# Optimization experiments

Measured on AMD Instinct MI355X. Metric: run time of the kernel, lower is better.

Reference implementation:

```python
import jax, jax.numpy as jnp
import numpy as np
from jax.ops import segment_sum, segment_max

N_NODES = 100000
N_EDGES = 1600000
IN, HID, OUT = 256, 64, 40
NEG_SLOPE = 0.2  # DGL GATConv default


def setup_inputs() -> dict:
    key = jax.random.key(0)
    ks = jax.random.split(key, 12)
    feat = jax.random.normal(ks[0], (N_NODES, IN), dtype=jnp.float32)
    src = jax.random.randint(ks[1], (N_EDGES,), 0, N_NODES)
    dst = jax.random.randint(ks[2], (N_EDGES,), 0, N_NODES)
    def xavier(k, shape):
        fan = sum(shape)
        return jax.random.normal(k, shape, dtype=jnp.float32) * jnp.sqrt(2.0 / fan)
    return {
        "feat": feat, "src": src, "dst": dst,
        "W1": xavier(ks[3], (IN, HID)),  "b1": jnp.zeros((HID,), jnp.float32),
        "al1": xavier(ks[4], (HID,)),    "ar1": xavier(ks[5], (HID,)),
        "W2": xavier(ks[6], (HID, OUT)), "b2": jnp.zeros((OUT,), jnp.float32),
        "al2": xavier(ks[7], (OUT,)),    "ar2": xavier(ks[8], (OUT,)),
    }


def gat_layer(x, W, b, attn_l, attn_r, src, dst, n):
    # z: [N, F_out] projected features
    z = x @ W
    el = z @ attn_l          # [N] source attention logits
    er = z @ attn_r          # [N] destination attention logits
    e = jax.nn.leaky_relu(el[src] + er[dst], NEG_SLOPE)  # [E]
    # segment (per-destination) softmax over incoming edges
    m = segment_max(e, dst, num_segments=n)              # [N]
    w = jnp.exp(e - m[dst])                              # [E]
    s = segment_sum(w, dst, num_segments=n)              # [N]
    alpha = w / s[dst]                                   # [E]
    # scatter-add aggregation of alpha * z[src]
    out = segment_sum(alpha[:, None] * z[src], dst, num_segments=n)
    return out + b


def reference(feat, src, dst, W1, b1, al1, ar1, W2, b2, al2, ar2):
    n = feat.shape[0]
    h = gat_layer(feat, W1, b1, al1, ar1, src, dst, n)
    h = jax.nn.relu(h)  # dropout is identity in eval mode
    h = gat_layer(h, W2, b2, al2, ar2, src, dst, n)
    return jax.nn.log_softmax(h, axis=-1)  # [N, out_size]
```

## Files before the change

### kernel.cpp

```cpp
#include <hip/hip_runtime.h>
#include <math.h>

constexpr int NN   = 100000;
constexpr int NE   = 1600000;
constexpr int FIN  = 256;
constexpr int HID  = 64;
constexpr int FOUT = 40;
constexpr float SLOPE = 0.2f;
constexpr int NB    = (NN + 255) / 256;
constexpr int NBUCK = NB;
constexpr int TILE_A = 2048;
constexpr int NWG_A = (NE + TILE_A - 1) / TILE_A;
constexpr int AK = 264;

typedef short  short8  __attribute__((ext_vector_type(8)));
typedef float  floatx4 __attribute__((ext_vector_type(4)));

__device__ inline unsigned short f2bf(float x) {
    union { float f; unsigned int u; } c; c.f = x;
    unsigned int u = c.u;
    return (unsigned short)((u + 0x7FFF + ((u >> 16) & 1)) >> 16);
}

__device__ inline float readlane_f(float v, int l) {
    return __int_as_float(__builtin_amdgcn_readlane(__float_as_int(v), l));
}

__global__ __launch_bounds__(256) void w1t_kernel(
    const float* __restrict__ W1, unsigned short* __restrict__ W1T)
{
    int idx = blockIdx.x * 256 + threadIdx.x;
    if (idx < FIN * HID) {
        int k = idx >> 6, n = idx & 63;
        W1T[n * FIN + k] = f2bf(W1[idx]);
    }
}

__global__ __launch_bounds__(256) void gemm1_kernel(
    const float* __restrict__ feat, const unsigned short* __restrict__ W1T,
    const float* __restrict__ al, const float* __restrict__ ar,
    const int* __restrict__ dst, int* __restrict__ bcnt,
    _Float16* __restrict__ z, float* __restrict__ el, float* __restrict__ er)
{
    __shared__ unsigned short sBT[64 * AK];
    __shared__ int hist[NBUCK];
    const int t = threadIdx.x;
    const int ntile = blockIdx.x * 64;

    for (int i = t; i < NBUCK; i += 256) hist[i] = 0;
    #pragma unroll
    for (int i = 0; i < 8; ++i) {
        int g = t + 256 * i;
        int row = g >> 5, c8 = g & 31;
        *(uint4*)&sBT[row * AK + 8 * c8] = *(const uint4*)&W1T[row * FIN + 8 * c8];
    }
    __syncthreads();

    {
        int base = (blockIdx.x * 256 + t) * 4;
        if (base < NE) {
            const int4 d4 = *(const int4*)&dst[base];
            atomicAdd(&hist[d4.x >> 8], 1); atomicAdd(&hist[d4.y >> 8], 1);
            atomicAdd(&hist[d4.z >> 8], 1); atomicAdd(&hist[d4.w >> 8], 1);
        }
    }
    __syncthreads();
    for (int i = t; i < NBUCK; i += 256) {
        int hv = hist[i];
        if (hv) atomicAdd(&bcnt[i], hv);
    }

    const int w  = t >> 6;
    const int l  = t & 63;
    const int lr = l & 15;
    const int q  = l >> 4;
    const int m0 = 16 * w;

    int n = ntile + m0 + lr; if (n >= NN) n = NN - 1;
    const float* __restrict__ arow = feat + (size_t)n * FIN;

    floatx4 acc[4];
    #pragma unroll
    for (int tile = 0; tile < 4; ++tile) acc[tile] = 0.f;

    #pragma unroll
    for (int kc = 0; kc < 8; ++kc) {
        const int koff = kc * 32 + 8 * q;
        const float4 fa = *(const float4*)(arow + koff);
        const float4 fb = *(const float4*)(arow + koff + 4);
        short8 av;
        av[0] = (short)f2bf(fa.x); av[1] = (short)f2bf(fa.y);
        av[2] = (short)f2bf(fa.z); av[3] = (short)f2bf(fa.w);
        av[4] = (short)f2bf(fb.x); av[5] = (short)f2bf(fb.y);
        av[6] = (short)f2bf(fb.z); av[7] = (short)f2bf(fb.w);
        #pragma unroll
        for (int tile = 0; tile < 4; ++tile) {
            const short8 bv = *(const short8*)(sBT + (16 * tile + lr) * AK + koff);
            acc[tile] = __builtin_amdgcn_mfma_f32_16x16x32_bf16(av, bv, acc[tile], 0, 0, 0);
        }
    }

    float aln[4], arn[4];
    #pragma unroll
    for (int tile = 0; tile < 4; ++tile) {
        aln[tile] = al[16 * tile + lr];
        arn[tile] = ar[16 * tile + lr];
    }
    #pragma unroll
    for (int r = 0; r < 4; ++r) {
        int mg = ntile + m0 + 4 * q + r;
        float pl = 0.f, pr = 0.f;
        #pragma unroll
        for (int tile = 0; tile < 4; ++tile) {
            float zv = acc[tile][r];
            pl += zv * aln[tile]; pr += zv * arn[tile];
        }
        #pragma unroll
        for (int off = 8; off >= 1; off >>= 1) {
            pl += __shfl_xor(pl, off);
            pr += __shfl_xor(pr, off);
        }
        if (mg < NN) {
            #pragma unroll
            for (int tile = 0; tile < 4; ++tile)
                z[(size_t)mg * HID + 16 * tile + lr] = (_Float16)acc[tile][r];
            if (lr == 0) { el[mg] = pl; er[mg] = pr; }
        }
    }
}

__global__ __launch_bounds__(512) void scan_top_kernel(
    const int* __restrict__ bcnt, int* __restrict__ bofs, int* __restrict__ gcur)
{
    __shared__ int tmp[512];
    int t = threadIdx.x;
    int v = (t < NB) ? bcnt[t] : 0;
    tmp[t] = v; __syncthreads();
    for (int off = 1; off < 512; off <<= 1) {
        int x = (t >= off) ? tmp[t - off] : 0;
        __syncthreads();
        tmp[t] += x;
        __syncthreads();
    }
    int excl = tmp[t] - v;
    if (t < NB) { bofs[t] = excl; gcur[t] = excl; }
    if (t == NB - 1) bofs[NB] = excl + v;
}

__global__ __launch_bounds__(1024) void partitionA_kernel(
    const int* __restrict__ src, const int* __restrict__ dst,
    int* __restrict__ gcur, int* __restrict__ ebuck)
{
    __shared__ int hist[NBUCK];
    __shared__ int lcur[NBUCK];
    const int t = threadIdx.x;
    const int e0 = blockIdx.x * TILE_A;
    const int e1 = (e0 + TILE_A < NE) ? e0 + TILE_A : NE;

    for (int i = t; i < NBUCK; i += 1024) hist[i] = 0;
    __syncthreads();
    for (int e = e0 + t; e < e1; e += 1024)
        atomicAdd(&hist[dst[e] >> 8], 1);
    __syncthreads();
    for (int i = t; i < NBUCK; i += 1024) {
        int hv = hist[i];
        lcur[i] = hv ? atomicAdd(&gcur[i], hv) : 0;
    }
    __syncthreads();
    for (int e = e0 + t; e < e1; e += 1024) {
        int d = dst[e], s = src[e];
        int p = atomicAdd(&lcur[d >> 8], 1);
        ebuck[p] = (s << 8) | (d & 255);
    }
}

__global__ __launch_bounds__(1024) void partitionB_kernel(
    const int* __restrict__ bofs, const int* __restrict__ ebuck,
    int* __restrict__ row_ptr, int* __restrict__ esrc)
{
    __shared__ int sdeg[256];
    __shared__ int sscan[256];
    __shared__ int scur[256];
    const int b = blockIdx.x;
    const int n0 = b << 8;
    const int t = threadIdx.x;
    const int r0 = bofs[b], r1 = bofs[b + 1];

    if (t < 256) sdeg[t] = 0;
    __syncthreads();
    for (int e = r0 + t; e < r1; e += 1024)
        atomicAdd(&sdeg[ebuck[e] & 255], 1);
    __syncthreads();

    if (t < 256) sscan[t] = sdeg[t];
    __syncthreads();
    for (int off = 1; off < 256; off <<= 1) {
        int x = 0;
        if (t < 256 && t >= off) x = sscan[t - off];
        __syncthreads();
        if (t < 256) sscan[t] += x;
        __syncthreads();
    }
    if (t < 256) {
        int excl = sscan[t] - sdeg[t];
        if (n0 + t < NN) row_ptr[n0 + t] = r0 + excl;
        scur[t] = r0 + excl;
    }
    if (b == NBUCK - 1 && t == 0) row_ptr[NN] = NE;
    __syncthreads();

    for (int e = r0 + t; e < r1; e += 1024) {
        int pk = ebuck[e];
        int p = atomicAdd(&scur[pk & 255], 1);
        esrc[p] = pk >> 8;
    }
}

template<int F, bool FINAL_LAYER>
__global__ __launch_bounds__(256) void gat_gather_kernel(
    const int* __restrict__ row_ptr, const int* __restrict__ esrc,
    const float* __restrict__ el, const float* __restrict__ er,
    const _Float16* __restrict__ z, const float* __restrict__ bias,
    const float* __restrict__ W2, const float* __restrict__ al2,
    const float* __restrict__ ar2,
    _Float16* __restrict__ z2, float* __restrict__ el2, float* __restrict__ er2,
    float* __restrict__ out)
{
    __shared__ float sW2[HID * FOUT];
    __shared__ float sh[4][HID];
    const int w = threadIdx.x >> 6, lane = threadIdx.x & 63;
    const int d = blockIdx.x * 4 + w;
    const int r0 = row_ptr[d], r1 = row_ptr[d + 1];
    const int cnt = r1 - r0;
    const float erd = er[d];

    if (!FINAL_LAYER) {
        for (int i = threadIdx.x; i < HID * FOUT; i += 256) sW2[i] = W2[i];
        __syncthreads();
    }

    float accv = 0.f;
    float s = 0.f;

    if (cnt <= 64) {
        int sn = 0; float v = -INFINITY;
        if (lane < cnt) {
            sn = esrc[r0 + lane];
            v = el[sn] + erd;
            v = (v >= 0.f) ? v : SLOPE * v;
        }
        float m = v;
        #pragma unroll
        for (int off = 32; off >= 1; off >>= 1) m = fmaxf(m, __shfl_xor(m, off));
        float wv = (lane < cnt) ? __expf(v - m) : 0.f;
        s = wv;
        #pragma unroll
        for (int off = 32; off >= 1; off >>= 1) s += __shfl_xor(s, off);
        if (lane < F) {
            int j = 0;
            for (; j + 8 <= cnt; j += 8) {
                float a0 = 0.f, a1 = 0.f;
                #pragma unroll
                for (int qq = 0; qq < 8; qq += 2) {
                    float w0 = readlane_f(wv, j + qq);
                    int   s0 = __builtin_amdgcn_readlane(sn, j + qq);
                    float w1 = readlane_f(wv, j + qq + 1);
                    int   s1 = __builtin_amdgcn_readlane(sn, j + qq + 1);
                    a0 += w0 * (float)z[(size_t)s0 * F + lane];
                    a1 += w1 * (float)z[(size_t)s1 * F + lane];
                }
                accv += a0 + a1;
            }
            for (; j < cnt; ++j) {
                float w0 = readlane_f(wv, j);
                int   s0 = __builtin_amdgcn_readlane(sn, j);
                accv += w0 * (float)z[(size_t)s0 * F + lane];
            }
        }
    } else {
        float m = -INFINITY;
        for (int e = r0 + lane; e < r1; e += 64) {
            float v = el[esrc[e]] + erd;
            v = (v >= 0.f) ? v : SLOPE * v;
            m = fmaxf(m, v);
        }
        #pragma unroll
        for (int off = 32; off >= 1; off >>= 1) m = fmaxf(m, __shfl_xor(m, off));
        for (int base = r0; base < r1; base += 64) {
            int e = base + lane;
            float wv = 0.f; int sn = 0;
            if (e < r1) {
                sn = esrc[e];
                float v = el[sn] + erd;
                v = (v >= 0.f) ? v : SLOPE * v;
                wv = __expf(v - m);
            }
            s += wv;
            int c = r1 - base; if (c > 64) c = 64;
            if (lane < F) {
                int j = 0;
                for (; j + 4 <= c; j += 4) {
                    float a0 = 0.f, a1 = 0.f;
                    #pragma unroll
                    for (int qq = 0; qq < 4; qq += 2) {
                        float w0 = readlane_f(wv, j + qq);
                        int   s0 = __builtin_amdgcn_readlane(sn, j + qq);
                        float w1 = readlane_f(wv, j + qq + 1);
                        int   s1 = __builtin_amdgcn_readlane(sn, j + qq + 1);
                        a0 += w0 * (float)z[(size_t)s0 * F + lane];
                        a1 += w1 * (float)z[(size_t)s1 * F + lane];
                    }
                    accv += a0 + a1;
                }
                for (; j < c; ++j) {
                    float w0 = readlane_f(wv, j);
                    int   s0 = __builtin_amdgcn_readlane(sn, j);
                    accv += w0 * (float)z[(size_t)s0 * F + lane];
                }
            }
        }
        #pragma unroll
        for (int off = 32; off >= 1; off >>= 1) s += __shfl_xor(s, off);
    }

    float res = (cnt > 0) ? (accv / s) : 0.f;

    if (!FINAL_LAYER) {
        float hval = res + bias[lane];
        hval = (hval > 0.f) ? hval : 0.f;
        sh[w][lane] = hval;
        float acc2 = 0.f;
        if (lane < FOUT) {
            #pragma unroll 8
            for (int k = 0; k < HID; ++k) acc2 += sh[w][k] * sW2[k * FOUT + lane];
        }
        float pl = (lane < FOUT) ? acc2 * al2[lane] : 0.f;
        float pr = (lane < FOUT) ? acc2 * ar2[lane] : 0.f;
        #pragma unroll
        for (int off = 32; off >= 1; off >>= 1) {
            pl += __shfl_xor(pl, off); pr += __shfl_xor(pr, off);
        }
        if (lane == 0) { el2[d] = pl; er2[d] = pr; }
        if (lane < FOUT) z2[(size_t)d * FOUT + lane] = (_Float16)acc2;
    } else {
        float v = (lane < F) ? res + bias[lane] : -INFINITY;
        float mx = v;
        #pragma unroll
        for (int off = 32; off >= 1; off >>= 1) mx = fmaxf(mx, __shfl_xor(mx, off));
        float ex = (lane < F) ? __expf(v - mx) : 0.f;
        float sm = ex;
        #pragma unroll
        for (int off = 32; off >= 1; off >>= 1) sm += __shfl_xor(sm, off);
        if (lane < F) out[(size_t)d * F + lane] = v - mx - __logf(sm);
    }
}

extern "C" void kernel_launch(void* const* d_in, const int* in_sizes, int n_in,
                              void* d_out, int out_size, void* d_ws, size_t ws_size,
                              hipStream_t stream) {
    const float* feat = (const float*)d_in[0];
    const int*   src  = (const int*)d_in[1];
    const int*   dst  = (const int*)d_in[2];
    const float* W1   = (const float*)d_in[3];
    const float* b1   = (const float*)d_in[4];
    const float* al1  = (const float*)d_in[5];
    const float* ar1  = (const float*)d_in[6];
    const float* W2   = (const float*)d_in[7];
    const float* b2   = (const float*)d_in[8];
    const float* al2  = (const float*)d_in[9];
    const float* ar2  = (const float*)d_in[10];
    float* out = (float*)d_out;

    char* p = (char*)d_ws;
    _Float16* z1 = (_Float16*)p;  p += (size_t)NN * HID * 2;
    _Float16* z2 = (_Float16*)p;  p += (size_t)NN * FOUT * 2;
    float* el1   = (float*)p;     p += (size_t)NN * 4;
    float* er1   = (float*)p;     p += (size_t)NN * 4;
    float* el2   = (float*)p;     p += (size_t)NN * 4;
    float* er2   = (float*)p;     p += (size_t)NN * 4;
    int*   bcnt  = (int*)p;       p += NB * 4;
    int*   bofs  = (int*)p;       p += (NB + 1) * 4;
    int*   gcur  = (int*)p;       p += NBUCK * 4;
    int*   rowp  = (int*)p;       p += (NN + 1) * 4;
    int*   esrc  = (int*)p;       p += (size_t)NE * 4;
    int*   ebuck = (int*)p;       p += (size_t)NE * 4;
    unsigned short* w1t = (unsigned short*)p;

    hipMemsetAsync(bcnt, 0, NB * sizeof(int), stream);

    w1t_kernel<<<(FIN * HID + 255) / 256, 256, 0, stream>>>(W1, w1t);
    gemm1_kernel<<<(NN + 63) / 64, 256, 0, stream>>>(feat, w1t, al1, ar1, dst, bcnt, z1, el1, er1);

    scan_top_kernel<<<1, 512, 0, stream>>>(bcnt, bofs, gcur);
    partitionA_kernel<<<NWG_A, 1024, 0, stream>>>(src, dst, gcur, ebuck);
    partitionB_kernel<<<NBUCK, 1024, 0, stream>>>(bofs, ebuck, rowp, esrc);

    gat_gather_kernel<HID, false><<<NN / 4, 256, 0, stream>>>(
        rowp, esrc, el1, er1, z1, b1, W2, al2, ar2, z2, el2, er2, nullptr);

    gat_gather_kernel<FOUT, true><<<NN / 4, 256, 0, stream>>>(
        rowp, esrc, el2, er2, z2, b2, nullptr, nullptr, nullptr,
        nullptr, nullptr, nullptr, out);
}
```

Before: 414.0 us.

## Reassociate layer-2 projection: aggregate hidden features before multiplying by W2

Layer 2 no longer projects h through W2 inside the first gather. Its attention logits come from h dotted with precomputed W2·al2 and W2·ar2 vectors, the second gather aggregates the 64-wide fp16 h, and a new out_kernel then applies W2, the bias and log_softmax. This drops the per-node shared W2 load and matmul from the first gather and the lane<F masking, at the cost of gathering 64 features instead of 40 in layer 2, an extra fp32 hagg write and read, and one more launch. hagg aliases the z1 buffer, which is safe because z1 is dead by then.

```diff
diff --git a/kernel.cpp b/kernel.cpp
--- a/kernel.cpp
+++ b/kernel.cpp
@@ -27,12 +27,25 @@
 }
 
 __global__ __launch_bounds__(256) void w1t_kernel(
-    const float* __restrict__ W1, unsigned short* __restrict__ W1T)
+    const float* __restrict__ W1, unsigned short* __restrict__ W1T,
+    const float* __restrict__ W2, const float* __restrict__ al2,
+    const float* __restrict__ ar2,
+    float* __restrict__ wl2, float* __restrict__ wr2)
 {
     int idx = blockIdx.x * 256 + threadIdx.x;
     if (idx < FIN * HID) {
         int k = idx >> 6, n = idx & 63;
         W1T[n * FIN + k] = f2bf(W1[idx]);
+    }
+    if (blockIdx.x == 0 && threadIdx.x < HID) {
+        int k = threadIdx.x;
+        float a = 0.f, b = 0.f;
+        #pragma unroll 8
+        for (int j = 0; j < FOUT; ++j) {
+            float wv = W2[k * FOUT + j];
+            a += wv * al2[j]; b += wv * ar2[j];
+        }
+        wl2[k] = a; wr2[k] = b;
     }
 }
 
@@ -216,28 +229,20 @@
     }
 }
 
-template<int F, bool FINAL_LAYER>
+template<bool FIRST>
 __global__ __launch_bounds__(256) void gat_gather_kernel(
     const int* __restrict__ row_ptr, const int* __restrict__ esrc,
     const float* __restrict__ el, const float* __restrict__ er,
-    const _Float16* __restrict__ z, const float* __restrict__ bias,
-    const float* __restrict__ W2, const float* __restrict__ al2,
-    const float* __restrict__ ar2,
-    _Float16* __restrict__ z2, float* __restrict__ el2, float* __restrict__ er2,
-    float* __restrict__ out)
-{
-    __shared__ float sW2[HID * FOUT];
-    __shared__ float sh[4][HID];
+    const _Float16* __restrict__ zin, const float* __restrict__ b1,
+    const float* __restrict__ wl2, const float* __restrict__ wr2,
+    _Float16* __restrict__ hout, float* __restrict__ haggout,
+    float* __restrict__ el2, float* __restrict__ er2)
+{
     const int w = threadIdx.x >> 6, lane = threadIdx.x & 63;
     const int d = blockIdx.x * 4 + w;
     const int r0 = row_ptr[d], r1 = row_ptr[d + 1];
     const int cnt = r1 - r0;
     const float erd = er[d];
-
-    if (!FINAL_LAYER) {
-        for (int i = threadIdx.x; i < HID * FOUT; i += 256) sW2[i] = W2[i];
-        __syncthreads();
-    }
 
     float accv = 0.f;
     float s = 0.f;
@@ -256,7 +261,7 @@
         s = wv;
         #pragma unroll
         for (int off = 32; off >= 1; off >>= 1) s += __shfl_xor(s, off);
-        if (lane < F) {
+        {
             int j = 0;
             for (; j + 8 <= cnt; j += 8) {
                 float a0 = 0.f, a1 = 0.f;
@@ -266,15 +271,15 @@
                     int   s0 = __builtin_amdgcn_readlane(sn, j + qq);
                     float w1 = readlane_f(wv, j + qq + 1);
                     int   s1 = __builtin_amdgcn_readlane(sn, j + qq + 1);
-                    a0 += w0 * (float)z[(size_t)s0 * F + lane];
-                    a1 += w1 * (float)z[(size_t)s1 * F + lane];
+                    a0 += w0 * (float)zin[(size_t)s0 * HID + lane];
+                    a1 += w1 * (float)zin[(size_t)s1 * HID + lane];
                 }
                 accv += a0 + a1;
             }
             for (; j < cnt; ++j) {
                 float w0 = readlane_f(wv, j);
                 int   s0 = __builtin_amdgcn_readlane(sn, j);
-                accv += w0 * (float)z[(size_t)s0 * F + lane];
+                accv += w0 * (float)zin[(size_t)s0 * HID + lane];
             }
         }
     } else {
@@ -297,7 +302,7 @@
             }
             s += wv;
             int c = r1 - base; if (c > 64) c = 64;
-            if (lane < F) {
+            {
                 int j = 0;
                 for (; j + 4 <= c; j += 4) {
                     float a0 = 0.f, a1 = 0.f;
@@ -307,15 +312,15 @@
                         int   s0 = __builtin_amdgcn_readlane(sn, j + qq);
                         float w1 = readlane_f(wv, j + qq + 1);
                         int   s1 = __builtin_amdgcn_readlane(sn, j + qq + 1);
-                        a0 += w0 * (float)z[(size_t)s0 * F + lane];
-                        a1 += w1 * (float)z[(size_t)s1 * F + lane];
+                        a0 += w0 * (float)zin[(size_t)s0 * HID + lane];
+                        a1 += w1 * (float)zin[(size_t)s1 * HID + lane];
                     }
                     accv += a0 + a1;
                 }
                 for (; j < c; ++j) {
                     float w0 = readlane_f(wv, j);
                     int   s0 = __builtin_amdgcn_readlane(sn, j);
-                    accv += w0 * (float)z[(size_t)s0 * F + lane];
+                    accv += w0 * (float)zin[(size_t)s0 * HID + lane];
                 }
             }
         }
@@ -325,34 +330,45 @@
 
     float res = (cnt > 0) ? (accv / s) : 0.f;
 
-    if (!FINAL_LAYER) {
-        float hval = res + bias[lane];
+    if (FIRST) {
+        float hval = res + b1[lane];
         hval = (hval > 0.f) ? hval : 0.f;
-        sh[w][lane] = hval;
-        float acc2 = 0.f;
-        if (lane < FOUT) {
-            #pragma unroll 8
-            for (int k = 0; k < HID; ++k) acc2 += sh[w][k] * sW2[k * FOUT + lane];
-        }
-        float pl = (lane < FOUT) ? acc2 * al2[lane] : 0.f;
-        float pr = (lane < FOUT) ? acc2 * ar2[lane] : 0.f;
+        hout[(size_t)d * HID + lane] = (_Float16)hval;
+        float pl = hval * wl2[lane];
+        float pr = hval * wr2[lane];
         #pragma unroll
         for (int off = 32; off >= 1; off >>= 1) {
             pl += __shfl_xor(pl, off); pr += __shfl_xor(pr, off);
         }
         if (lane == 0) { el2[d] = pl; er2[d] = pr; }
-        if (lane < FOUT) z2[(size_t)d * FOUT + lane] = (_Float16)acc2;
     } else {
-        float v = (lane < F) ? res + bias[lane] : -INFINITY;
-        float mx = v;
-        #pragma unroll
-        for (int off = 32; off >= 1; off >>= 1) mx = fmaxf(mx, __shfl_xor(mx, off));
-        float ex = (lane < F) ? __expf(v - mx) : 0.f;
-        float sm = ex;
-        #pragma unroll
-        for (int off = 32; off >= 1; off >>= 1) sm += __shfl_xor(sm, off);
-        if (lane < F) out[(size_t)d * F + lane] = v - mx - __logf(sm);
-    }
+        haggout[(size_t)d * HID + lane] = res;
+    }
+}
+
+__global__ __launch_bounds__(256) void out_kernel(
+    const float* __restrict__ hagg, const float* __restrict__ W2,
+    const float* __restrict__ b2, float* __restrict__ out)
+{
+    __shared__ float sh[4][64];
+    const int w = threadIdx.x >> 6, lane = threadIdx.x & 63;
+    const int n = blockIdx.x * 4 + w;
+    sh[w][lane] = hagg[(size_t)n * HID + lane];
+    __syncthreads();
+    float acc = 0.f;
+    if (lane < FOUT) {
+        #pragma unroll 8
+        for (int k = 0; k < HID; ++k) acc += sh[w][k] * W2[k * FOUT + lane];
+    }
+    float v = (lane < FOUT) ? acc + b2[lane] : -INFINITY;
+    float mx = v;
+    #pragma unroll
+    for (int off = 32; off >= 1; off >>= 1) mx = fmaxf(mx, __shfl_xor(mx, off));
+    float ex = (lane < FOUT) ? __expf(v - mx) : 0.f;
+    float sm = ex;
+    #pragma unroll
+    for (int off = 32; off >= 1; off >>= 1) sm += __shfl_xor(sm, off);
+    if (lane < FOUT) out[(size_t)n * FOUT + lane] = v - mx - __logf(sm);
 }
 
 extern "C" void kernel_launch(void* const* d_in, const int* in_sizes, int n_in,
@@ -372,12 +388,15 @@
     float* out = (float*)d_out;
 
     char* p = (char*)d_ws;
-    _Float16* z1 = (_Float16*)p;  p += (size_t)NN * HID * 2;
-    _Float16* z2 = (_Float16*)p;  p += (size_t)NN * FOUT * 2;
+    float*    hagg = (float*)p;
+    _Float16* z1   = (_Float16*)p;  p += (size_t)NN * HID * 4;
+    _Float16* h    = (_Float16*)p;  p += (size_t)NN * HID * 2;
     float* el1   = (float*)p;     p += (size_t)NN * 4;
     float* er1   = (float*)p;     p += (size_t)NN * 4;
     float* el2   = (float*)p;     p += (size_t)NN * 4;
     float* er2   = (float*)p;     p += (size_t)NN * 4;
+    float* wl2   = (float*)p;     p += HID * 4;
+    float* wr2   = (float*)p;     p += HID * 4;
     int*   bcnt  = (int*)p;       p += NB * 4;
     int*   bofs  = (int*)p;       p += (NB + 1) * 4;
     int*   gcur  = (int*)p;       p += NBUCK * 4;
@@ -388,17 +407,20 @@
 
     hipMemsetAsync(bcnt, 0, NB * sizeof(int), stream);
 
-    w1t_kernel<<<(FIN * HID + 255) / 256, 256, 0, stream>>>(W1, w1t);
+    w1t_kernel<<<(FIN * HID + 255) / 256, 256, 0, stream>>>(
+        W1, w1t, W2, al2, ar2, wl2, wr2);
     gemm1_kernel<<<(NN + 63) / 64, 256, 0, stream>>>(feat, w1t, al1, ar1, dst, bcnt, z1, el1, er1);
 
     scan_top_kernel<<<1, 512, 0, stream>>>(bcnt, bofs, gcur);
     partitionA_kernel<<<NWG_A, 1024, 0, stream>>>(src, dst, gcur, ebuck);
     partitionB_kernel<<<NBUCK, 1024, 0, stream>>>(bofs, ebuck, rowp, esrc);
 
-    gat_gather_kernel<HID, false><<<NN / 4, 256, 0, stream>>>(
-        rowp, esrc, el1, er1, z1, b1, W2, al2, ar2, z2, el2, er2, nullptr);
-
-    gat_gather_kernel<FOUT, true><<<NN / 4, 256, 0, stream>>>(
-        rowp, esrc, el2, er2, z2, b2, nullptr, nullptr, nullptr,
-        nullptr, nullptr, nullptr, out);
-}
+    gat_gather_kernel<true><<<NN / 4, 256, 0, stream>>>(
+        rowp, esrc, el1, er1, z1, b1, wl2, wr2, h, nullptr, el2, er2);
+
+    gat_gather_kernel<false><<<NN / 4, 256, 0, stream>>>(
+        rowp, esrc, el2, er2, h, nullptr, nullptr, nullptr,
+        nullptr, hagg, nullptr, nullptr);
+
+    out_kernel<<<NN / 4, 256, 0, stream>>>(hagg, W2, b2, out);
+}
```

After: 418.3 us. About the same (+1.0%).
